# Kernel tuning notes

Hardware: AMD Instinct MI355X
Metric: run time of the kernel (lower is better)

Reference implementation:

```python
import jax, jax.numpy as jnp
import numpy as np

B, T, I, H, O = 128, 512, 512, 2048, 512  # batch, seq_length, input, hidden, output


def setup_inputs() -> dict:
    key = jax.random.key(0)
    ks = jax.random.split(key, 8)
    s_ih = 1.0 / np.sqrt(H)  # torch RNNCell/Linear default init scale 1/sqrt(hidden)
    body = jax.random.normal(ks[0], (B, T - 1, I), dtype=jnp.float32)
    # last timestep row stores the integer pad index (as float), per the module's protocol
    pad = jax.random.randint(ks[1], (B,), 0, T - 2)
    last = jnp.broadcast_to(pad[:, None, None].astype(jnp.float32), (B, 1, I))
    x = jnp.concatenate([body, last], axis=1)  # [B, T, I]
    W_ih = jax.random.uniform(ks[2], (H, I), jnp.float32, -s_ih, s_ih)
    W_hh = jax.random.uniform(ks[3], (H, H), jnp.float32, -s_ih, s_ih)
    b_ih = jax.random.uniform(ks[4], (H,), jnp.float32, -s_ih, s_ih)
    b_hh = jax.random.uniform(ks[5], (H,), jnp.float32, -s_ih, s_ih)
    W_fc = jax.random.uniform(ks[6], (O, H), jnp.float32, -s_ih, s_ih)
    b_fc = jax.random.uniform(ks[7], (O,), jnp.float32, -s_ih, s_ih)
    h0 = jnp.ones((H,), jnp.float32)  # self.h parameter, ones-initialized
    return {"x": x, "h0": h0, "W_ih": W_ih, "b_ih": b_ih, "W_hh": W_hh,
            "b_hh": b_hh, "W_fc": W_fc, "b_fc": b_fc}


def reference(x, h0, W_ih, b_ih, W_hh, b_hh, W_fc, b_fc):
    steps = T - 2  # loop runs over x.shape[2]-1 = (T-1)-1 timesteps
    pad = x[:, -1, 0].astype(jnp.int32)          # [B] pad indices
    xs = jnp.transpose(x[:, :steps, :], (1, 0, 2))  # [steps, B, I]
    h_init = jnp.broadcast_to(h0, (x.shape[0], H))  # self.h * ones([B,1])

    def step(h, xt):
        h = jnp.tanh(xt @ W_ih.T + b_ih + h @ W_hh.T + b_hh)
        return h, h @ W_fc.T + b_fc

    _, outs = jax.lax.scan(step, h_init, xs)     # [steps, B, O]
    # mask selects the single timestep j == pad_len[b]; everything else is zeroed
    mask = (pad[None, :] == jnp.arange(steps)[:, None]).astype(outs.dtype)  # [steps, B]
    return jnp.sum(outs * mask[:, :, None], axis=0)  # [B, O]
```

## Files before the change

kernel.cpp:

```cpp
#include <hip/hip_runtime.h>

#define Bsz 128
#define Tsz 512
#define Isz 512
#define Hsz 2048
#define Osz 512
#define STEPS 510

typedef short short8 __attribute__((ext_vector_type(8)));
typedef float floatx4 __attribute__((ext_vector_type(4)));

__device__ __forceinline__ unsigned short f2bf(float f) {
  unsigned int u = __builtin_bit_cast(unsigned int, f);
  u += 0x7FFFu + ((u >> 16) & 1u);
  return (unsigned short)(u >> 16);
}

__device__ __forceinline__ float tanh_fast(float x) {
  const float e = __expf(2.f * x);
  return 1.f - 2.f * __builtin_amdgcn_rcpf(e + 1.f);
}

template <int AUX>
__device__ __forceinline__ void gload_lds16(const void* g, void* l) {
  __builtin_amdgcn_global_load_lds(
      (const __attribute__((address_space(1))) void*)g,
      (__attribute__((address_space(3))) void*)l, 16, 0, AUX);
}

__global__ __launch_bounds__(256, 1)
void rnn_kernel(const float* __restrict__ x, const float* __restrict__ h0v,
                const float* __restrict__ W_ih, const float* __restrict__ b_ih,
                const float* __restrict__ W_hh, const float* __restrict__ b_hh,
                unsigned short* __restrict__ hbuf,
                float* __restrict__ hfinal,
                unsigned int* __restrict__ flags,
                unsigned int* __restrict__ xcc_arr)
{
  __shared__ short h_lds[4 * 8192];
  __shared__ float red_lds[4 * 1024];
  __shared__ int pad_lds[16];
  __shared__ unsigned int mode_lds;

  const int tid = threadIdx.x;
  const int lane = tid & 63;
  const int wv = tid >> 6;
  const int m16 = lane & 15;
  const int quad = lane >> 4;
  const int m7 = m16 & 7;
  const int rg = blockIdx.x & 7;
  const int cg = blockIdx.x >> 3;
  const int b0 = rg * 16;
  const int c0 = cg * 64;
  const int kq = wv * 512;
  const int kqx = wv * 128;
  const int wvoff = wv * 8192;

  {
    unsigned int xcc;
    asm volatile("s_getreg_b32 %0, hwreg(HW_REG_XCC_ID)" : "=s"(xcc));
    if (tid == 0)
      __hip_atomic_store(&xcc_arr[rg * 32 + cg], xcc + 1u, __ATOMIC_RELAXED,
                         __HIP_MEMORY_SCOPE_AGENT);
    if (wv == 0) {
      const unsigned int* ap = &xcc_arr[rg * 32 + (lane & 31)];
      unsigned int v;
      do {
        v = __hip_atomic_load(ap, __ATOMIC_RELAXED, __HIP_MEMORY_SCOPE_AGENT);
        if (__all((int)(v != 0u))) break;
        __builtin_amdgcn_s_sleep(2);
      } while (true);
      const int same = __all((int)(v == xcc + 1u));
      if (tid == 0) mode_lds = (unsigned int)same;
    }
  }

  short8 wf[16][4];
  short8 wih[4][4];
#pragma unroll
  for (int nt = 0; nt < 4; ++nt) {
    const int wrow = c0 + nt * 16 + m16;
    const float* base = W_hh + (size_t)wrow * Hsz + kq + quad * 8;
#pragma unroll
    for (int kc = 0; kc < 16; ++kc) {
      short8 v;
#pragma unroll
      for (int j = 0; j < 8; ++j) v[j] = (short)f2bf(base[kc * 32 + j]);
      wf[kc][nt] = v;
    }
    const float* basex = W_ih + (size_t)wrow * Isz + kqx + quad * 8;
#pragma unroll
    for (int kc = 0; kc < 4; ++kc) {
      short8 v;
#pragma unroll
      for (int j = 0; j < 8; ++j) v[j] = (short)f2bf(basex[kc * 32 + j]);
      wih[kc][nt] = v;
    }
  }

  const int rrow = tid >> 4;
  const int rcb = (tid & 15) * 4;
  float bias[4];
#pragma unroll
  for (int i = 0; i < 4; ++i) bias[i] = b_ih[c0 + rcb + i] + b_hh[c0 + rcb + i];

  if (tid < 16)
    pad_lds[tid] = (int)x[(size_t)(b0 + tid) * (Tsz * Isz) + (size_t)(Tsz - 1) * Isz];

  for (int i = lane; i < 1024; i += 64) {
    const int c = i >> 7;
    const int r = (i >> 3) & 15;
    const int u = i & 7;
    const int k = kq + c * 64 + u * 8;
    short8 v;
#pragma unroll
    for (int j = 0; j < 8; ++j) v[j] = (short)f2bf(h0v[k + j]);
    *reinterpret_cast<short8*>(&h_lds[wvoff + c * 1024 + r * 64 + (u ^ (r & 7)) * 8]) = v;
  }

  __syncthreads();
  const bool use_l2 = (mode_lds != 0u);

  const unsigned int* fp = flags + (size_t)(wv * 8 + (lane & 7)) * 8 + rg;

  for (int t = 0; t < STEPS; ++t) {
    const bool have_next = (t + 1) < STEPS;

    const float* xp = x + (size_t)(b0 + m16) * (Tsz * Isz) + (size_t)t * Isz + kqx + quad * 8;
    float4 xv[8];
#pragma unroll
    for (int kcc = 0; kcc < 4; ++kcc) {
      xv[2 * kcc] = *reinterpret_cast<const float4*>(xp + kcc * 32);
      xv[2 * kcc + 1] = *reinterpret_cast<const float4*>(xp + kcc * 32 + 4);
    }

    if (t > 0) {
      while (!__all((int)(__hip_atomic_load(fp, __ATOMIC_RELAXED,
                                            __HIP_MEMORY_SCOPE_AGENT) >= (unsigned)t)))
        __builtin_amdgcn_s_sleep(1);
      const unsigned short* hsrcp = hbuf + (size_t)(t & 1) * (Bsz * Hsz);
      if (use_l2) {
#pragma unroll
        for (int c = 0; c < 8; ++c) {
          const unsigned short* src = hsrcp + (size_t)((wv * 8 + c) * 8 + rg) * 1024;
          gload_lds16<0x01>(src + lane * 8, &h_lds[wvoff + c * 1024]);
          gload_lds16<0x01>(src + 512 + lane * 8, &h_lds[wvoff + c * 1024 + 512]);
        }
      } else {
#pragma unroll
        for (int c = 0; c < 8; ++c) {
          const unsigned short* src = hsrcp + (size_t)((wv * 8 + c) * 8 + rg) * 1024;
          gload_lds16<0x11>(src + lane * 8, &h_lds[wvoff + c * 1024]);
          gload_lds16<0x11>(src + 512 + lane * 8, &h_lds[wvoff + c * 1024 + 512]);
        }
      }
    }

    short8 xa[4];
#pragma unroll
    for (int kcc = 0; kcc < 4; ++kcc) {
      short8 a;
      a[0] = (short)f2bf(xv[2 * kcc].x);
      a[1] = (short)f2bf(xv[2 * kcc].y);
      a[2] = (short)f2bf(xv[2 * kcc].z);
      a[3] = (short)f2bf(xv[2 * kcc].w);
      a[4] = (short)f2bf(xv[2 * kcc + 1].x);
      a[5] = (short)f2bf(xv[2 * kcc + 1].y);
      a[6] = (short)f2bf(xv[2 * kcc + 1].z);
      a[7] = (short)f2bf(xv[2 * kcc + 1].w);
      xa[kcc] = a;
    }

    floatx4 acc[4];
#pragma unroll
    for (int nt = 0; nt < 4; ++nt) {
      floatx4 zero = {0.f, 0.f, 0.f, 0.f};
      acc[nt] = zero;
    }
#pragma unroll
    for (int kcc = 0; kcc < 4; ++kcc)
#pragma unroll
      for (int nt = 0; nt < 4; ++nt)
        acc[nt] = __builtin_amdgcn_mfma_f32_16x16x32_bf16(xa[kcc], wih[kcc][nt], acc[nt], 0, 0, 0);

    __builtin_amdgcn_s_waitcnt(0x0F78);
#pragma unroll
    for (int c = 0; c < 4; ++c) {
      const int base = wvoff + c * 1024 + m16 * 64;
#pragma unroll
      for (int k2 = 0; k2 < 2; ++k2) {
        const short8 a =
            *reinterpret_cast<const short8*>(&h_lds[base + ((k2 * 4 + quad) ^ m7) * 8]);
#pragma unroll
        for (int nt = 0; nt < 4; ++nt)
          acc[nt] = __builtin_amdgcn_mfma_f32_16x16x32_bf16(a, wf[c * 2 + k2][nt], acc[nt], 0, 0, 0);
      }
    }
    __builtin_amdgcn_s_waitcnt(0x0F70);
#pragma unroll
    for (int c = 4; c < 8; ++c) {
      const int base = wvoff + c * 1024 + m16 * 64;
#pragma unroll
      for (int k2 = 0; k2 < 2; ++k2) {
        const short8 a =
            *reinterpret_cast<const short8*>(&h_lds[base + ((k2 * 4 + quad) ^ m7) * 8]);
#pragma unroll
        for (int nt = 0; nt < 4; ++nt)
          acc[nt] = __builtin_amdgcn_mfma_f32_16x16x32_bf16(a, wf[c * 2 + k2][nt], acc[nt], 0, 0, 0);
      }
    }

#pragma unroll
    for (int nt = 0; nt < 4; ++nt)
#pragma unroll
      for (int i = 0; i < 4; ++i)
        red_lds[wv * 1024 + (quad * 4 + i) * 64 + nt * 16 + m16] = acc[nt][i];

    __syncthreads();

    {
      float4 z = {0.f, 0.f, 0.f, 0.f};
#pragma unroll
      for (int ww = 0; ww < 4; ++ww) {
        const float4 p =
            *reinterpret_cast<const float4*>(&red_lds[ww * 1024 + rrow * 64 + rcb]);
        z.x += p.x; z.y += p.y; z.z += p.z; z.w += p.w;
      }
      const float t0 = tanh_fast(z.x + bias[0]);
      const float t1 = tanh_fast(z.y + bias[1]);
      const float t2 = tanh_fast(z.z + bias[2]);
      const float t3 = tanh_fast(z.w + bias[3]);
      unsigned long long pk = (unsigned long long)f2bf(t0) |
                              ((unsigned long long)f2bf(t1) << 16) |
                              ((unsigned long long)f2bf(t2) << 32) |
                              ((unsigned long long)f2bf(t3) << 48);
      const int toff = rrow * 64 + ((rcb >> 3) ^ (rrow & 7)) * 8 + ((rcb >> 2) & 1) * 4;
      unsigned short* hd = hbuf + (size_t)((t + 1) & 1) * (Bsz * Hsz) +
                           (size_t)(cg * 8 + rg) * 1024 + toff;
      if (use_l2) {
        *reinterpret_cast<unsigned long long*>(hd) = pk;
      } else {
        __hip_atomic_store(reinterpret_cast<unsigned long long*>(hd), pk,
                           __ATOMIC_RELAXED, __HIP_MEMORY_SCOPE_AGENT);
      }
      if (pad_lds[rrow] == t) {
        float4 o;
        o.x = t0; o.y = t1; o.z = t2; o.w = t3;
        *reinterpret_cast<float4*>(&hfinal[(size_t)(b0 + rrow) * Hsz + c0 + rcb]) = o;
      }
    }

    __syncthreads();

    if (have_next && tid == 0) {
      __hip_atomic_store(flags + cg * 8 + rg, (unsigned)(t + 1),
                         __ATOMIC_RELAXED, __HIP_MEMORY_SCOPE_AGENT);
    }
  }
}

__global__ __launch_bounds__(64)
void fc_kernel(const float* __restrict__ hfinal, const float* __restrict__ W_fc,
               const float* __restrict__ b_fc, float* __restrict__ out) {
  const int lane = threadIdx.x & 63;
  const int m16 = lane & 15;
  const int quad = lane >> 4;
  const int b0 = (blockIdx.x & 7) * 16;
  const int o0 = (blockIdx.x >> 3) * 16;
  floatx4 acc = {0.f, 0.f, 0.f, 0.f};
  const float* ap = hfinal + (size_t)(b0 + m16) * Hsz + quad * 8;
  const float* bp = W_fc + (size_t)(o0 + m16) * Hsz + quad * 8;
#pragma unroll 4
  for (int kc = 0; kc < 64; ++kc) {
    short8 a, b;
#pragma unroll
    for (int j = 0; j < 8; ++j) a[j] = (short)f2bf(ap[kc * 32 + j]);
#pragma unroll
    for (int j = 0; j < 8; ++j) b[j] = (short)f2bf(bp[kc * 32 + j]);
    acc = __builtin_amdgcn_mfma_f32_16x16x32_bf16(a, b, acc, 0, 0, 0);
  }
  const float bias = b_fc[o0 + m16];
#pragma unroll
  for (int i = 0; i < 4; ++i)
    out[(size_t)(b0 + quad * 4 + i) * Osz + o0 + m16] = acc[i] + bias;
}

__global__ void zero_flags(unsigned int* f) { f[blockIdx.x * 256 + threadIdx.x] = 0u; }

extern "C" void kernel_launch(void* const* d_in, const int* in_sizes, int n_in,
                              void* d_out, int out_size, void* d_ws, size_t ws_size,
                              hipStream_t stream) {
  const float* x = (const float*)d_in[0];
  const float* h0 = (const float*)d_in[1];
  const float* W_ih = (const float*)d_in[2];
  const float* b_ih = (const float*)d_in[3];
  const float* W_hh = (const float*)d_in[4];
  const float* b_hh = (const float*)d_in[5];
  const float* W_fc = (const float*)d_in[6];
  const float* b_fc = (const float*)d_in[7];
  float* out = (float*)d_out;

  char* ws = (char*)d_ws;
  unsigned short* hbuf = (unsigned short*)ws;
  float* hfinal = (float*)(ws + (1u << 20));
  unsigned int* flags = (unsigned int*)(ws + (2u << 20));
  unsigned int* xcc_arr = flags + 256;

  zero_flags<<<2, 256, 0, stream>>>(flags);
  rnn_kernel<<<256, 256, 0, stream>>>(x, h0, W_ih, b_ih, W_hh, b_hh, hbuf, hfinal,
                                      flags, xcc_arr);
  fc_kernel<<<256, 64, 0, stream>>>(hfinal, W_fc, b_fc, out);
}
```

Before: 2.074 ms.

## Move input-projection MFMAs before flag wait and pipeline per-chunk h loads

Issues the x·W_ih MFMAs before spinning on the inter-block step flags, so that work overlaps with waiting for the previous hidden state. The h-to-LDS loads are then consumed chunk by chunk with finer vmcnt waits, and LDS reads are double-buffered against the MFMAs. The aim is to shorten the serial critical path of each recurrence step. The finer waits rely on in-order vmcnt counting and add register pressure.

```diff
diff --git a/kernel.cpp b/kernel.cpp
--- a/kernel.cpp
+++ b/kernel.cpp
@@ -27,6 +27,25 @@
       (const __attribute__((address_space(1))) void*)g,
       (__attribute__((address_space(3))) void*)l, 16, 0, AUX);
 }
+
+#define HLOAD(c, enc, A, B)                                                             \
+  {                                                                                     \
+    __builtin_amdgcn_s_waitcnt(enc);                                                    \
+    const int hb = wvoff + (c) * 1024 + m16 * 64;                                       \
+    A = *reinterpret_cast<const short8*>(&h_lds[hb + (quad ^ m7) * 8]);                 \
+    B = *reinterpret_cast<const short8*>(&h_lds[hb + ((4 + quad) ^ m7) * 8]);           \
+  }
+#define HMFMA(c, A, B)                                                                  \
+  {                                                                                     \
+    acc[0] = __builtin_amdgcn_mfma_f32_16x16x32_bf16(A, wf[(c) * 2][0], acc[0], 0, 0, 0);  \
+    acc[1] = __builtin_amdgcn_mfma_f32_16x16x32_bf16(A, wf[(c) * 2][1], acc[1], 0, 0, 0);  \
+    acc[2] = __builtin_amdgcn_mfma_f32_16x16x32_bf16(A, wf[(c) * 2][2], acc[2], 0, 0, 0);  \
+    acc[3] = __builtin_amdgcn_mfma_f32_16x16x32_bf16(A, wf[(c) * 2][3], acc[3], 0, 0, 0);  \
+    acc[0] = __builtin_amdgcn_mfma_f32_16x16x32_bf16(B, wf[(c) * 2 + 1][0], acc[0], 0, 0, 0); \
+    acc[1] = __builtin_amdgcn_mfma_f32_16x16x32_bf16(B, wf[(c) * 2 + 1][1], acc[1], 0, 0, 0); \
+    acc[2] = __builtin_amdgcn_mfma_f32_16x16x32_bf16(B, wf[(c) * 2 + 1][2], acc[2], 0, 0, 0); \
+    acc[3] = __builtin_amdgcn_mfma_f32_16x16x32_bf16(B, wf[(c) * 2 + 1][3], acc[3], 0, 0, 0); \
+  }
 
 __global__ __launch_bounds__(256, 1)
 void rnn_kernel(const float* __restrict__ x, const float* __restrict__ h0v,
@@ -133,29 +152,6 @@
       xv[2 * kcc] = *reinterpret_cast<const float4*>(xp + kcc * 32);
       xv[2 * kcc + 1] = *reinterpret_cast<const float4*>(xp + kcc * 32 + 4);
     }
-
-    if (t > 0) {
-      while (!__all((int)(__hip_atomic_load(fp, __ATOMIC_RELAXED,
-                                            __HIP_MEMORY_SCOPE_AGENT) >= (unsigned)t)))
-        __builtin_amdgcn_s_sleep(1);
-      const unsigned short* hsrcp = hbuf + (size_t)(t & 1) * (Bsz * Hsz);
-      if (use_l2) {
-#pragma unroll
-        for (int c = 0; c < 8; ++c) {
-          const unsigned short* src = hsrcp + (size_t)((wv * 8 + c) * 8 + rg) * 1024;
-          gload_lds16<0x01>(src + lane * 8, &h_lds[wvoff + c * 1024]);
-          gload_lds16<0x01>(src + 512 + lane * 8, &h_lds[wvoff + c * 1024 + 512]);
-        }
-      } else {
-#pragma unroll
-        for (int c = 0; c < 8; ++c) {
-          const unsigned short* src = hsrcp + (size_t)((wv * 8 + c) * 8 + rg) * 1024;
-          gload_lds16<0x11>(src + lane * 8, &h_lds[wvoff + c * 1024]);
-          gload_lds16<0x11>(src + 512 + lane * 8, &h_lds[wvoff + c * 1024 + 512]);
-        }
-      }
-    }
-
     short8 xa[4];
 #pragma unroll
     for (int kcc = 0; kcc < 4; ++kcc) {
@@ -170,7 +166,6 @@
       a[7] = (short)f2bf(xv[2 * kcc + 1].w);
       xa[kcc] = a;
     }
-
     floatx4 acc[4];
 #pragma unroll
     for (int nt = 0; nt < 4; ++nt) {
@@ -183,31 +178,46 @@
       for (int nt = 0; nt < 4; ++nt)
         acc[nt] = __builtin_amdgcn_mfma_f32_16x16x32_bf16(xa[kcc], wih[kcc][nt], acc[nt], 0, 0, 0);
 
-    __builtin_amdgcn_s_waitcnt(0x0F78);
-#pragma unroll
-    for (int c = 0; c < 4; ++c) {
-      const int base = wvoff + c * 1024 + m16 * 64;
-#pragma unroll
-      for (int k2 = 0; k2 < 2; ++k2) {
-        const short8 a =
-            *reinterpret_cast<const short8*>(&h_lds[base + ((k2 * 4 + quad) ^ m7) * 8]);
-#pragma unroll
-        for (int nt = 0; nt < 4; ++nt)
-          acc[nt] = __builtin_amdgcn_mfma_f32_16x16x32_bf16(a, wf[c * 2 + k2][nt], acc[nt], 0, 0, 0);
+    if (t > 0) {
+      while (!__all((int)(__hip_atomic_load(fp, __ATOMIC_RELAXED,
+                                            __HIP_MEMORY_SCOPE_AGENT) >= (unsigned)t)))
+        __builtin_amdgcn_s_sleep(1);
+      const unsigned short* hsrcp = hbuf + (size_t)(t & 1) * (Bsz * Hsz);
+      if (use_l2) {
+#pragma unroll
+        for (int c = 0; c < 8; ++c) {
+          const unsigned short* src = hsrcp + (size_t)((wv * 8 + c) * 8 + rg) * 1024;
+          gload_lds16<0x01>(src + lane * 8, &h_lds[wvoff + c * 1024]);
+          gload_lds16<0x01>(src + 512 + lane * 8, &h_lds[wvoff + c * 1024 + 512]);
+        }
+      } else {
+#pragma unroll
+        for (int c = 0; c < 8; ++c) {
+          const unsigned short* src = hsrcp + (size_t)((wv * 8 + c) * 8 + rg) * 1024;
+          gload_lds16<0x11>(src + lane * 8, &h_lds[wvoff + c * 1024]);
+          gload_lds16<0x11>(src + 512 + lane * 8, &h_lds[wvoff + c * 1024 + 512]);
+        }
       }
     }
-    __builtin_amdgcn_s_waitcnt(0x0F70);
-#pragma unroll
-    for (int c = 4; c < 8; ++c) {
-      const int base = wvoff + c * 1024 + m16 * 64;
-#pragma unroll
-      for (int k2 = 0; k2 < 2; ++k2) {
-        const short8 a =
-            *reinterpret_cast<const short8*>(&h_lds[base + ((k2 * 4 + quad) ^ m7) * 8]);
-#pragma unroll
-        for (int nt = 0; nt < 4; ++nt)
-          acc[nt] = __builtin_amdgcn_mfma_f32_16x16x32_bf16(a, wf[c * 2 + k2][nt], acc[nt], 0, 0, 0);
-      }
+
+    {
+      short8 A0, B0, A1, B1;
+      HLOAD(0, 0x0F7E, A0, B0)
+      HLOAD(1, 0x0F7C, A1, B1)
+      HMFMA(0, A0, B0)
+      HLOAD(2, 0x0F7A, A0, B0)
+      HMFMA(1, A1, B1)
+      HLOAD(3, 0x0F78, A1, B1)
+      HMFMA(2, A0, B0)
+      HLOAD(4, 0x0F76, A0, B0)
+      HMFMA(3, A1, B1)
+      HLOAD(5, 0x0F74, A1, B1)
+      HMFMA(4, A0, B0)
+      HLOAD(6, 0x0F72, A0, B0)
+      HMFMA(5, A1, B1)
+      HLOAD(7, 0x0F70, A1, B1)
+      HMFMA(6, A0, B0)
+      HMFMA(7, A1, B1)
     }
 
 #pragma unroll
```

New measurement: 2.691 ms. 29.8% more time.
